# Performance work log

Hardware: AMD Instinct MI355X
Metric: run time of the kernel (lower is better)

The kernel has to match this reference:

```python
import jax, jax.numpy as jnp
import numpy as np


def setup_inputs() -> dict:
    key = jax.random.key(0)
    k1, k2 = jax.random.split(key)
    B, C, H, W = 16, 3, 512, 512
    predicted = jax.random.normal(k1, (B, C, H, W), dtype=jnp.float32)
    target = jax.random.randint(k2, (B, H, W), 0, 3, dtype=jnp.int32)
    return {"predicted": predicted, "target": target, "num_classes": 3}


def reference(predicted, target, num_classes):
    # predicted: [B, C, H, W] logits; target: [B, H, W] int labels
    B, C, H, W = predicted.shape
    smooth = 1.0

    # F.cross_entropy with default 'mean' reduction over all pixels
    logp = jax.nn.log_softmax(predicted, axis=1)           # [B,C,H,W]
    ce = -jnp.mean(jnp.take_along_axis(logp, target[:, None, :, :], axis=1))

    # Dice: the original casts softmax probs with .long() before summing,
    # which truncates toward zero (probs in [0,1) -> 0, exactly 1.0 -> 1).
    # We reproduce that faithfully with jnp.trunc.
    probs = jnp.exp(logp).reshape(B, C, H * W)             # softmax probs, [B,C,HW]
    tp = jnp.trunc(probs)                                   # faithful to .long() cast
    tgt = target.reshape(B, H * W)
    onehot = (tgt[:, None, :] == jnp.arange(num_classes)[None, :, None]).astype(probs.dtype)  # [B,nc,HW]

    intersection = jnp.sum(tp[:, :num_classes, :] * onehot, axis=-1)                 # [B,nc]
    union = jnp.sum(tp[:, :num_classes, :], axis=-1) + jnp.sum(onehot, axis=-1)      # [B,nc]
    coef = (2.0 * intersection + smooth) / (union + smooth)                           # [B,nc]
    batch_dice = jnp.mean(coef)  # mean over classes then batch == mean over both

    return ce + 1.0 - batch_dice
```

## Files before the change

### kernel.cpp

```cpp
#include <hip/hip_runtime.h>

constexpr int B_   = 16;
constexpr int C_   = 3;
constexpr int HW_  = 512 * 512;
constexpr int THREADS = 256;
constexpr int BLOCKS_PER_IMG = 64;
constexpr int NBLOCKS = B_ * BLOCKS_PER_IMG;
constexpr int F4_PER_BLOCK = HW_ / 4 / BLOCKS_PER_IMG;
constexpr int ITERS = F4_PER_BLOCK / THREADS;
constexpr int REC = 12;


__global__ __launch_bounds__(THREADS) void dice_ce_partial(
    const float* __restrict__ pred, const int* __restrict__ tgt,
    float* __restrict__ ws) {
  const int b = blockIdx.x / BLOCKS_PER_IMG;
  const int j = blockIdx.x % BLOCKS_PER_IMG;
  const int t = threadIdx.x;

  const float4* p0 = (const float4*)(pred + (size_t)b * C_ * HW_);
  const float4* p1 = (const float4*)(pred + (size_t)b * C_ * HW_ + HW_);
  const float4* p2 = (const float4*)(pred + (size_t)b * C_ * HW_ + 2 * HW_);
  const int4*   tg = (const int4*)(tgt + (size_t)b * HW_);

  float4 A0[ITERS], A1[ITERS], A2[ITERS];
  int4   T[ITERS];
#pragma unroll
  for (int i = 0; i < ITERS; ++i) {
    const int idx = j * F4_PER_BLOCK + i * THREADS + t;
    A0[i] = p0[idx];
    A1[i] = p1[idx];
    A2[i] = p2[idx];
    T[i]  = tg[idx];
  }

  float ce = 0.f;
  float cnt[3] = {0.f, 0.f, 0.f};
  float tps[3] = {0.f, 0.f, 0.f};
  float itr[3] = {0.f, 0.f, 0.f};

#pragma unroll
  for (int i = 0; i < ITERS; ++i) {
    float x0s[4] = {A0[i].x, A0[i].y, A0[i].z, A0[i].w};
    float x1s[4] = {A1[i].x, A1[i].y, A1[i].z, A1[i].w};
    float x2s[4] = {A2[i].x, A2[i].y, A2[i].z, A2[i].w};
    int   tvs[4] = {T[i].x, T[i].y, T[i].z, T[i].w};
#pragma unroll
    for (int k = 0; k < 4; ++k) {
      float x0 = x0s[k], x1 = x1s[k], x2 = x2s[k];
      int tv = tvs[k];
      float m  = fmaxf(x0, fmaxf(x1, x2));
      float e0 = __expf(x0 - m), e1 = __expf(x1 - m), e2 = __expf(x2 - m);
      float s  = e0 + e1 + e2;
      float ls = __logf(s);
      float xt = (tv == 0) ? x0 : ((tv == 1) ? x1 : x2);
      ce += (m + ls) - xt;
      cnt[0] += (tv == 0) ? 1.f : 0.f;
      cnt[1] += (tv == 1) ? 1.f : 0.f;
      cnt[2] += (tv == 2) ? 1.f : 0.f;
      float t0 = (e0 >= s) ? 1.f : 0.f;
      float t1 = (e1 >= s) ? 1.f : 0.f;
      float t2 = (e2 >= s) ? 1.f : 0.f;
      tps[0] += t0; tps[1] += t1; tps[2] += t2;
      float tt_ = (tv == 0) ? t0 : ((tv == 1) ? t1 : t2);
      itr[0] += (tv == 0) ? tt_ : 0.f;
      itr[1] += (tv == 1) ? tt_ : 0.f;
      itr[2] += (tv == 2) ? tt_ : 0.f;
    }
  }

  float vals[10] = {ce, cnt[0], cnt[1], cnt[2], tps[0], tps[1], tps[2],
                    itr[0], itr[1], itr[2]};
#pragma unroll
  for (int k = 0; k < 10; ++k) {
    float v = vals[k];
#pragma unroll
    for (int off = 32; off > 0; off >>= 1) v += __shfl_down(v, off, 64);
    vals[k] = v;
  }

  __shared__ float red[THREADS / 64][10];
  const int wave = t >> 6, lane = t & 63;
  if (lane == 0) {
#pragma unroll
    for (int k = 0; k < 10; ++k) red[wave][k] = vals[k];
  }
  __syncthreads();
  if (t == 0) {
#pragma unroll
    for (int k = 0; k < 10; ++k) {
      float s = red[0][k];
#pragma unroll
      for (int w = 1; w < THREADS / 64; ++w) s += red[w][k];
      vals[k] = s;
    }
    float4* rec = (float4*)(ws + (size_t)blockIdx.x * REC);
    rec[0] = make_float4(vals[0], vals[1], vals[2], vals[3]);
    rec[1] = make_float4(vals[4], vals[5], vals[6], vals[7]);
    rec[2] = make_float4(vals[8], vals[9], 0.f, 0.f);
  }
}

__global__ __launch_bounds__(1024) void dice_ce_final(
    const float* __restrict__ ws, float* __restrict__ out) {
  const int t = threadIdx.x;
  const int img = t >> 6;
  const int lane = t & 63;

  const float4* rec = (const float4*)(ws + (size_t)(img * 64 + lane) * REC);
  float4 r0 = rec[0], r1 = rec[1], r2 = rec[2];
  float v[10] = {r0.x, r0.y, r0.z, r0.w, r1.x, r1.y, r1.z, r1.w, r2.x, r2.y};
#pragma unroll
  for (int k = 0; k < 10; ++k) {
#pragma unroll
    for (int off = 32; off > 0; off >>= 1) v[k] += __shfl_down(v[k], off, 64);
  }

  __shared__ float ceS[16];
  __shared__ float coefS[16];
  if (lane == 0) {
    float coef = (2.f * v[7] + 1.f) / (v[4] + v[1] + 1.f)
               + (2.f * v[8] + 1.f) / (v[5] + v[2] + 1.f)
               + (2.f * v[9] + 1.f) / (v[6] + v[3] + 1.f);
    ceS[img] = v[0];
    coefS[img] = coef;
  }
  __syncthreads();
  if (t == 0) {
    float ce = 0.f, cf = 0.f;
#pragma unroll
    for (int i = 0; i < 16; ++i) { ce += ceS[i]; cf += coefS[i]; }
    out[0] = ce / ((float)B_ * (float)HW_) + 1.f - cf / (float)(B_ * C_);
  }
}

extern "C" void kernel_launch(void* const* d_in, const int* in_sizes, int n_in,
                              void* d_out, int out_size, void* d_ws, size_t ws_size,
                              hipStream_t stream) {
  const float* pred = (const float*)d_in[0];
  const int*   tgt  = (const int*)d_in[1];
  float*       out  = (float*)d_out;
  float*       ws   = (float*)d_ws;

  dice_ce_partial<<<NBLOCKS, THREADS, 0, stream>>>(pred, tgt, ws);
  dice_ce_final<<<1, 1024, 0, stream>>>(ws, out);
}
```

Measured before the change: 99.32 us.

## Pack dice counters into 16-bit integer lanes and double blocks per image

Replaces the nine float dice counters with four int accumulators, each holding two 16-bit counts. The class-0 count is derived in the final kernel as HW minus the other two counts. This cuts ALU work and the number of cross-lane shuffles in the partial reduction. Blocks per image go from 64 to 128, halving registers per thread and raising parallelism, and the final kernel now sums two records per lane. Per-block counts must stay below 65536, which holds at 2048 pixels per block.

```diff
diff --git a/kernel.cpp b/kernel.cpp
--- a/kernel.cpp
+++ b/kernel.cpp
@@ -4,11 +4,11 @@
 constexpr int C_   = 3;
 constexpr int HW_  = 512 * 512;
 constexpr int THREADS = 256;
-constexpr int BLOCKS_PER_IMG = 64;
+constexpr int BLOCKS_PER_IMG = 128;
 constexpr int NBLOCKS = B_ * BLOCKS_PER_IMG;
 constexpr int F4_PER_BLOCK = HW_ / 4 / BLOCKS_PER_IMG;
 constexpr int ITERS = F4_PER_BLOCK / THREADS;
-constexpr int REC = 12;
+constexpr int REC = 8;
 
 
 __global__ __launch_bounds__(THREADS) void dice_ce_partial(
@@ -35,9 +35,7 @@
   }
 
   float ce = 0.f;
-  float cnt[3] = {0.f, 0.f, 0.f};
-  float tps[3] = {0.f, 0.f, 0.f};
-  float itr[3] = {0.f, 0.f, 0.f};
+  int pkA = 0, pkB = 0, pkC = 0, pkD = 0;
 
 #pragma unroll
   for (int i = 0; i < ITERS; ++i) {
@@ -55,49 +53,44 @@
       float ls = __logf(s);
       float xt = (tv == 0) ? x0 : ((tv == 1) ? x1 : x2);
       ce += (m + ls) - xt;
-      cnt[0] += (tv == 0) ? 1.f : 0.f;
-      cnt[1] += (tv == 1) ? 1.f : 0.f;
-      cnt[2] += (tv == 2) ? 1.f : 0.f;
-      float t0 = (e0 >= s) ? 1.f : 0.f;
-      float t1 = (e1 >= s) ? 1.f : 0.f;
-      float t2 = (e2 >= s) ? 1.f : 0.f;
-      tps[0] += t0; tps[1] += t1; tps[2] += t2;
-      float tt_ = (tv == 0) ? t0 : ((tv == 1) ? t1 : t2);
-      itr[0] += (tv == 0) ? tt_ : 0.f;
-      itr[1] += (tv == 1) ? tt_ : 0.f;
-      itr[2] += (tv == 2) ? tt_ : 0.f;
+      int t0 = (e0 >= s) ? 1 : 0;
+      int t1 = (e1 >= s) ? 1 : 0;
+      int t2 = (e2 >= s) ? 1 : 0;
+      pkA += ((tv == 1) ? 1 : 0) + ((tv == 2) ? (1 << 16) : 0);
+      pkB += t0 + (t1 << 16);
+      pkC += t2 + (((tv == 0) ? t0 : 0) << 16);
+      pkD += ((tv == 1) ? t1 : 0) + (((tv == 2) ? t2 : 0) << 16);
     }
   }
 
-  float vals[10] = {ce, cnt[0], cnt[1], cnt[2], tps[0], tps[1], tps[2],
-                    itr[0], itr[1], itr[2]};
+  int pks[4] = {pkA, pkB, pkC, pkD};
 #pragma unroll
-  for (int k = 0; k < 10; ++k) {
-    float v = vals[k];
+  for (int off = 32; off > 0; off >>= 1) {
+    ce += __shfl_down(ce, off, 64);
 #pragma unroll
-    for (int off = 32; off > 0; off >>= 1) v += __shfl_down(v, off, 64);
-    vals[k] = v;
+    for (int k = 0; k < 4; ++k) pks[k] += __shfl_down(pks[k], off, 64);
   }
 
-  __shared__ float red[THREADS / 64][10];
+  __shared__ float ceR[THREADS / 64];
+  __shared__ int   pkR[THREADS / 64][4];
   const int wave = t >> 6, lane = t & 63;
   if (lane == 0) {
+    ceR[wave] = ce;
 #pragma unroll
-    for (int k = 0; k < 10; ++k) red[wave][k] = vals[k];
+    for (int k = 0; k < 4; ++k) pkR[wave][k] = pks[k];
   }
   __syncthreads();
   if (t == 0) {
 #pragma unroll
-    for (int k = 0; k < 10; ++k) {
-      float s = red[0][k];
+    for (int w = 1; w < THREADS / 64; ++w) {
+      ce += ceR[w];
 #pragma unroll
-      for (int w = 1; w < THREADS / 64; ++w) s += red[w][k];
-      vals[k] = s;
+      for (int k = 0; k < 4; ++k) pks[k] += pkR[w][k];
     }
     float4* rec = (float4*)(ws + (size_t)blockIdx.x * REC);
-    rec[0] = make_float4(vals[0], vals[1], vals[2], vals[3]);
-    rec[1] = make_float4(vals[4], vals[5], vals[6], vals[7]);
-    rec[2] = make_float4(vals[8], vals[9], 0.f, 0.f);
+    rec[0] = make_float4(ce, __int_as_float(pks[0]), __int_as_float(pks[1]),
+                         __int_as_float(pks[2]));
+    rec[1] = make_float4(__int_as_float(pks[3]), 0.f, 0.f, 0.f);
   }
 }
 
@@ -107,11 +100,26 @@
   const int img = t >> 6;
   const int lane = t & 63;
 
-  const float4* rec = (const float4*)(ws + (size_t)(img * 64 + lane) * REC);
-  float4 r0 = rec[0], r1 = rec[1], r2 = rec[2];
-  float v[10] = {r0.x, r0.y, r0.z, r0.w, r1.x, r1.y, r1.z, r1.w, r2.x, r2.y};
+  float ce = 0.f;
+  float cnt1 = 0.f, cnt2 = 0.f;
+  float tps0 = 0.f, tps1 = 0.f, tps2 = 0.f;
+  float itr0 = 0.f, itr1 = 0.f, itr2 = 0.f;
 #pragma unroll
-  for (int k = 0; k < 10; ++k) {
+  for (int r = 0; r < 2; ++r) {
+    const int idx = img * BLOCKS_PER_IMG + r * 64 + lane;
+    const float4* rec = (const float4*)(ws + (size_t)idx * REC);
+    float4 r0 = rec[0], r1 = rec[1];
+    ce += r0.x;
+    int pA = __float_as_int(r0.y), pB = __float_as_int(r0.z);
+    int pC = __float_as_int(r0.w), pD = __float_as_int(r1.x);
+    cnt1 += (float)(pA & 0xffff); cnt2 += (float)(pA >> 16);
+    tps0 += (float)(pB & 0xffff); tps1 += (float)(pB >> 16);
+    tps2 += (float)(pC & 0xffff); itr0 += (float)(pC >> 16);
+    itr1 += (float)(pD & 0xffff); itr2 += (float)(pD >> 16);
+  }
+  float v[9] = {ce, cnt1, cnt2, tps0, tps1, tps2, itr0, itr1, itr2};
+#pragma unroll
+  for (int k = 0; k < 9; ++k) {
 #pragma unroll
     for (int off = 32; off > 0; off >>= 1) v[k] += __shfl_down(v[k], off, 64);
   }
@@ -119,18 +127,20 @@
   __shared__ float ceS[16];
   __shared__ float coefS[16];
   if (lane == 0) {
-    float coef = (2.f * v[7] + 1.f) / (v[4] + v[1] + 1.f)
-               + (2.f * v[8] + 1.f) / (v[5] + v[2] + 1.f)
-               + (2.f * v[9] + 1.f) / (v[6] + v[3] + 1.f);
+    float c1 = v[1], c2 = v[2];
+    float c0 = (float)HW_ - c1 - c2;
+    float coef = (2.f * v[6] + 1.f) / (v[3] + c0 + 1.f)
+               + (2.f * v[7] + 1.f) / (v[4] + c1 + 1.f)
+               + (2.f * v[8] + 1.f) / (v[5] + c2 + 1.f);
     ceS[img] = v[0];
     coefS[img] = coef;
   }
   __syncthreads();
   if (t == 0) {
-    float ce = 0.f, cf = 0.f;
+    float cesum = 0.f, cf = 0.f;
 #pragma unroll
-    for (int i = 0; i < 16; ++i) { ce += ceS[i]; cf += coefS[i]; }
-    out[0] = ce / ((float)B_ * (float)HW_) + 1.f - cf / (float)(B_ * C_);
+    for (int i = 0; i < 16; ++i) { cesum += ceS[i]; cf += coefS[i]; }
+    out[0] = cesum / ((float)B_ * (float)HW_) + 1.f - cf / (float)(B_ * C_);
   }
 }
 
```

New measurement: 96.97 us, median of 2. 2.4% less time.
